# Optimization experiments

Measured on AMD Instinct MI355X. Metric: run time of the kernel, lower is better.

Reference implementation:

```python
import jax, jax.numpy as jnp
import numpy as np

N, E, D, L = 100000, 400000, 300, 5
BN_EPS = 1e-5


def setup_inputs() -> dict:
    key = jax.random.key(0)
    ks = jax.random.split(key, 8)
    x = jax.random.randint(ks[0], (N, 7), 0, 5)
    edge_index = jax.random.randint(ks[1], (2, E), 0, N)
    edge_attr = jax.random.randint(ks[2], (E, 4), 0, 2)
    s = 0.1
    atom_tables = jax.random.normal(ks[3], (7, 119, D), jnp.float32) * s
    bond_tables = jax.random.normal(ks[4], (L, 4, 6, D), jnp.float32) * s
    mlp_w1 = jax.random.normal(ks[5], (L, D, 2 * D), jnp.float32) * (1.0 / np.sqrt(D))
    mlp_b1 = jnp.zeros((L, 2 * D), jnp.float32)
    mlp_w2 = jax.random.normal(ks[6], (L, 2 * D, D), jnp.float32) * (1.0 / np.sqrt(2 * D))
    mlp_b2 = jnp.zeros((L, D), jnp.float32)
    bn_gamma = jnp.ones((L, D), jnp.float32)
    bn_beta = jnp.zeros((L, D), jnp.float32)
    return dict(x=x, edge_index=edge_index, edge_attr=edge_attr,
                atom_tables=atom_tables, bond_tables=bond_tables,
                mlp_w1=mlp_w1, mlp_b1=mlp_b1, mlp_w2=mlp_w2, mlp_b2=mlp_b2,
                bn_gamma=bn_gamma, bn_beta=bn_beta)


def reference(x, edge_index, edge_attr, atom_tables, bond_tables,
              mlp_w1, mlp_b1, mlp_w2, mlp_b2, bn_gamma, bn_beta):
    n = x.shape[0]
    # add self loops (PyG add_self_loops appends them)
    loop = jnp.arange(n)
    src = jnp.concatenate([edge_index[0], loop])  # message source j
    dst = jnp.concatenate([edge_index[1], loop])  # aggregation target i
    self_loop_attr = jnp.zeros((n, 4), edge_attr.dtype).at[:, 0].set(4)
    ea = jnp.concatenate([edge_attr, self_loop_attr], axis=0)  # [E+N, 4]

    # AtomEncoder: sum of 7 per-feature embeddings -> [N, D]
    h = atom_tables[jnp.arange(7), x].sum(axis=1)

    for l in range(L):
        # BondEncoder: sum of 4 per-feature embeddings -> [E+N, D]
        e_emb = bond_tables[l][jnp.arange(4), ea].sum(axis=1)
        # GIN message = x_j + edge_emb, aggr='add' by target node
        msg = h[src] + e_emb
        agg = jax.ops.segment_sum(msg, dst, num_segments=n)
        # GIN update MLP: Linear -> ReLU -> Linear
        hid = jax.nn.relu(agg @ mlp_w1[l] + mlp_b1[l])
        out = hid @ mlp_w2[l] + mlp_b2[l]
        # BatchNorm1d (training mode: batch stats, biased var)
        mu = out.mean(axis=0)
        var = out.var(axis=0)
        out = (out - mu) / jnp.sqrt(var + BN_EPS) * bn_gamma[l] + bn_beta[l]
        # drop_ratio = 0.0 -> dropout is identity; ReLU except last layer
        if l < L - 1:
            out = jax.nn.relu(out)
        h = out
    return h  # JK='last'
```

## Files before the change

kernel.cpp:

```cpp
#include <hip/hip_runtime.h>

typedef unsigned short u16;
typedef unsigned int   u32;
typedef __bf16 bf16x8 __attribute__((ext_vector_type(8)));
typedef float  f32x4  __attribute__((ext_vector_type(4)));

__device__ __forceinline__ u16 f2bf(float f) {
    u32 u = __builtin_bit_cast(u32, f);
    u = u + 0x7fffu + ((u >> 16) & 1u);
    return (u16)(u >> 16);
}
__device__ __forceinline__ float bflo(u32 u) { return __builtin_bit_cast(float, u << 16); }
__device__ __forceinline__ float bfhi(u32 u) { return __builtin_bit_cast(float, u & 0xffff0000u); }
__device__ __forceinline__ u32 pack2(float x, float y) { return (u32)f2bf(x) | ((u32)f2bf(y) << 16); }

#define NN 100000
#define EE 400000
#define DP 320
#define HP 640

__global__ void count_deg(const int* __restrict__ ei, int* __restrict__ deg, int E) {
    int e = blockIdx.x * 256 + threadIdx.x;
    if (e < E) atomicAdd(&deg[ei[E + e]], 1);
}

__global__ void scan1(const int* __restrict__ deg, int* __restrict__ out, int* __restrict__ bsums, int n) {
    __shared__ int lds[1024];
    int t = threadIdx.x;
    int i = blockIdx.x * 1024 + t;
    int v = (i < n) ? deg[i] : 0;
    lds[t] = v;
    __syncthreads();
    for (int d = 1; d < 1024; d <<= 1) {
        int add = (t >= d) ? lds[t - d] : 0;
        __syncthreads();
        lds[t] += add;
        __syncthreads();
    }
    if (i < n) out[i] = lds[t] - v;
    if (t == 1023) bsums[blockIdx.x] = lds[t];
}

__global__ void scan2(int* __restrict__ bsums, int nb) {
    __shared__ int lds[128];
    int t = threadIdx.x;
    int v = (t < nb) ? bsums[t] : 0;
    lds[t] = v;
    __syncthreads();
    for (int d = 1; d < 128; d <<= 1) {
        int add = (t >= d) ? lds[t - d] : 0;
        __syncthreads();
        lds[t] += add;
        __syncthreads();
    }
    if (t < nb) bsums[t] = lds[t] - v;
}

__global__ void scan3(int* __restrict__ out, const int* __restrict__ bsums, int n, int etot) {
    int i = blockIdx.x * 1024 + threadIdx.x;
    if (i < n) out[i] += bsums[blockIdx.x];
    else if (i == n) out[i] = etot;
}

__global__ void fill_csr(const int* __restrict__ ei, const int* __restrict__ ea,
                         int* __restrict__ cursors, u32* __restrict__ vals, int E) {
    int e = blockIdx.x * 256 + threadIdx.x;
    if (e >= E) return;
    int dst = ei[E + e];
    int src = ei[e];
    u32 code = (u32)((ea[e*4] & 1) | ((ea[e*4+1] & 1) << 1) | ((ea[e*4+2] & 1) << 2) | ((ea[e*4+3] & 1) << 3));
    int pos = atomicAdd(&cursors[dst], 1);
    vals[pos] = ((u32)src << 4) | code;
}

__global__ void conv_w1(const float* __restrict__ w, u16* __restrict__ wt) {
    int id = blockIdx.x * 256 + threadIdx.x;
    if (id >= 5 * HP * DP) return;
    int l = id / (HP * DP);
    int rem = id - l * (HP * DP);
    int n = rem / DP;
    int k = rem - n * DP;
    u16 v = 0;
    if (n < 600 && k < 300) v = f2bf(w[((size_t)l * 300 + k) * 600 + n]);
    wt[id] = v;
}
__global__ void conv_w2(const float* __restrict__ w, u16* __restrict__ wt) {
    int id = blockIdx.x * 256 + threadIdx.x;
    if (id >= 5 * DP * HP) return;
    int l = id / (DP * HP);
    int rem = id - l * (DP * HP);
    int n = rem / HP;
    int k = rem - n * HP;
    u16 v = 0;
    if (n < 300 && k < 600) v = f2bf(w[((size_t)l * 600 + k) * 300 + n]);
    wt[id] = v;
}

__global__ void atom_enc(const int* __restrict__ x, const float* __restrict__ at, u16* __restrict__ y) {
    const int i = blockIdx.x;
    const int d = threadIdx.x;
    __shared__ int xi[7];
    if (d < 7) xi[d] = x[i * 7 + d];
    __syncthreads();
    u16 v = 0;
    if (d < 300) {
        float s = 0.f;
        #pragma unroll
        for (int f = 0; f < 7; ++f) s += at[(f * 119 + xi[f]) * 300 + d];
        v = f2bf(s);
    }
    y[(size_t)i * DP + d] = v;
}

__global__ void bond_enc(const float* __restrict__ bt, float* __restrict__ emb) {
    const int c = blockIdx.x;
    const int d = threadIdx.x;
    float s = 0.f;
    if (d < 300) {
        if (c < 16) {
            #pragma unroll
            for (int f = 0; f < 4; ++f) s += bt[(f * 6 + ((c >> f) & 1)) * 300 + d];
        } else {
            s = bt[4 * 300 + d];
            #pragma unroll
            for (int f = 1; f < 4; ++f) s += bt[f * 6 * 300 + d];
        }
    }
    emb[c * DP + d] = s;
}

__global__ void bn_ss(const float* __restrict__ stats, const float* __restrict__ gamma,
                      const float* __restrict__ beta, float* __restrict__ scale,
                      float* __restrict__ shift, int n) {
    int d = threadIdx.x;
    float sc = 0.f, sh = 0.f;
    if (d < 300) {
        float inv_n = 1.0f / (float)n;
        float mu = stats[d] * inv_n;
        float var = stats[DP + d] * inv_n - mu * mu;
        float inv = 1.0f / sqrtf(var + 1e-5f);
        sc = gamma[d] * inv;
        sh = beta[d] - mu * sc;
    }
    scale[d] = sc; shift[d] = sh;
}

__global__ void bn_apply(const float* __restrict__ hraw, const float* __restrict__ scale,
                         const float* __restrict__ shift, u16* __restrict__ y) {
    const int i = blockIdx.x;
    const int d = threadIdx.x;
    float v = fmaf(scale[d], hraw[(size_t)i * DP + d], shift[d]);
    y[(size_t)i * DP + d] = f2bf(fmaxf(v, 0.f));
}

__global__ void aggregate(const u16* __restrict__ y,
                          const float* __restrict__ emb,
                          const int* __restrict__ offs, const u32* __restrict__ vals,
                          u16* __restrict__ agg, const int n) {
    const int wid = (int)((blockIdx.x * (size_t)blockDim.x + threadIdx.x) >> 6);
    const int lane = threadIdx.x & 63;
    if (wid >= n) return;
    const int j0 = lane, j1 = lane + 64, j2 = lane + 128;
    const bool has2 = (lane < 32);

    float a0x = 0.f, a0y = 0.f, a1x = 0.f, a1y = 0.f, a2x = 0.f, a2y = 0.f;

    auto accum = [&](int srcrow, const float* erow) {
        const u32* row = (const u32*)y + (size_t)srcrow * (DP / 2);
        u32 u0 = row[j0], u1 = row[j1];
        u32 u2 = has2 ? row[j2] : 0u;
        float2 e0 = *(const float2*)(erow + 2 * j0);
        float2 e1 = *(const float2*)(erow + 2 * j1);
        a0x += bflo(u0) + e0.x;  a0y += bfhi(u0) + e0.y;
        a1x += bflo(u1) + e1.x;  a1y += bfhi(u1) + e1.y;
        if (has2) {
            float2 e2 = *(const float2*)(erow + 2 * j2);
            a2x += bflo(u2) + e2.x;  a2y += bfhi(u2) + e2.y;
        }
    };

    accum(wid, emb + 16 * DP);
    const int s = offs[wid], t = offs[wid + 1];
    for (int e = s; e < t; ++e) {
        u32 v = vals[e];
        accum((int)(v >> 4), emb + (v & 15u) * DP);
    }

    u32* out = (u32*)agg + (size_t)wid * (DP / 2);
    out[j0] = pack2(a0x, a0y);
    out[j1] = pack2(a1x, a1y);
    if (has2) out[j2] = pack2(a2x, a2y);
}

#define ASTR 328
#define HSTR 40

__global__ __launch_bounds__(512, 2) void fused_mlp(
    const u16* __restrict__ A,
    const u16* __restrict__ W1t,
    const u16* __restrict__ W2t,
    const float* __restrict__ b1g,
    const float* __restrict__ b2g,
    float* __restrict__ H,
    float* __restrict__ st1, float* __restrict__ st2,
    const int M) {

    __shared__ __align__(16) u16 As[128 * ASTR];
    __shared__ __align__(16) u16 Wb[2][320 * HSTR];
    __shared__ __align__(16) u16 hidT[128 * HSTR];

    const int tid  = threadIdx.x;
    const int bm   = blockIdx.x * 128;
    const int wave = tid >> 6;
    const int lane = tid & 63;
    const int mg   = wave >> 1;
    const int ng   = wave & 1;
    const int l15  = lane & 15;
    const int q    = lane >> 4;

    #pragma unroll
    for (int it = 0; it < 10; ++it) {
        int u = tid + it * 512;
        int row = u / 40, ku = u - row * 40;
        uint4 v; v.x = v.y = v.z = v.w = 0;
        if (bm + row < M) v = *(const uint4*)(A + (size_t)(bm + row) * DP + ku * 8);
        *(uint4*)&As[row * ASTR + ku * 8] = v;
    }
    {
        uint4 w0 = *(const uint4*)(W1t + (size_t)(tid / 40) * DP + (tid % 40) * 8);
        uint4 w1v = *(const uint4*)(W1t + (size_t)((tid + 512) / 40) * DP + ((tid + 512) % 40) * 8);
        uint4 w2v; w2v.x = w2v.y = w2v.z = w2v.w = 0;
        int u2 = tid + 1024;
        if (u2 < 1280) w2v = *(const uint4*)(W1t + (size_t)(u2 / 40) * DP + (u2 % 40) * 8);
        *(uint4*)&Wb[0][(tid / 40) * ASTR + (tid % 40) * 8] = w0;
        *(uint4*)&Wb[0][((tid + 512) / 40) * ASTR + ((tid + 512) % 40) * 8] = w1v;
        if (u2 < 1280) *(uint4*)&Wb[0][(u2 / 40) * ASTR + (u2 % 40) * 8] = w2v;
    }
    __syncthreads();

    bf16x8 afr[2][10];
    #pragma unroll
    for (int mf = 0; mf < 2; ++mf)
        #pragma unroll
        for (int kt = 0; kt < 10; ++kt) {
            uint4 t = *(const uint4*)&As[(mg * 32 + mf * 16 + l15) * ASTR + kt * 32 + q * 8];
            afr[mf][kt] = __builtin_bit_cast(bf16x8, t);
        }

    f32x4 acc2[2][10];
    const f32x4 zero4 = {0.f, 0.f, 0.f, 0.f};
    #pragma unroll
    for (int mf = 0; mf < 2; ++mf)
        #pragma unroll
        for (int nf = 0; nf < 10; ++nf) acc2[mf][nf] = zero4;

    for (int c = 0; c < 20; ++c) {
        uint4 p0, p1, p2;
        {
            int u0 = tid, u1 = tid + 512, u2 = tid + 1024;
            p0 = *(const uint4*)(W2t + (size_t)(u0 >> 2) * HP + c * 32 + (u0 & 3) * 8);
            p1 = *(const uint4*)(W2t + (size_t)(u1 >> 2) * HP + c * 32 + (u1 & 3) * 8);
            p2.x = p2.y = p2.z = p2.w = 0;
            if (u2 < 1280) p2 = *(const uint4*)(W2t + (size_t)(u2 >> 2) * HP + c * 32 + (u2 & 3) * 8);
        }

        f32x4 acc1[2] = {zero4, zero4};
        #pragma unroll
        for (int kt = 0; kt < 10; ++kt) {
            uint4 t = *(const uint4*)&Wb[0][(ng * 16 + l15) * ASTR + kt * 32 + q * 8];
            bf16x8 bfr = __builtin_bit_cast(bf16x8, t);
            acc1[0] = __builtin_amdgcn_mfma_f32_16x16x32_bf16(afr[0][kt], bfr, acc1[0], 0, 0, 0);
            acc1[1] = __builtin_amdgcn_mfma_f32_16x16x32_bf16(afr[1][kt], bfr, acc1[1], 0, 0, 0);
        }
        {
            int gcol = c * 32 + ng * 16 + l15;
            float bb = (gcol < 600) ? b1g[gcol] : 0.f;
            #pragma unroll
            for (int mf = 0; mf < 2; ++mf)
                #pragma unroll
                for (int r = 0; r < 4; ++r) {
                    float v = fmaxf(acc1[mf][r] + bb, 0.f);
                    hidT[(mg * 32 + mf * 16 + q * 4 + r) * HSTR + ng * 16 + l15] = f2bf(v);
                }
        }
        {
            int u0 = tid, u1 = tid + 512, u2 = tid + 1024;
            *(uint4*)&Wb[1][(u0 >> 2) * HSTR + (u0 & 3) * 8] = p0;
            *(uint4*)&Wb[1][(u1 >> 2) * HSTR + (u1 & 3) * 8] = p1;
            if (u2 < 1280) *(uint4*)&Wb[1][(u2 >> 2) * HSTR + (u2 & 3) * 8] = p2;
        }
        __syncthreads();

        uint4 q0, q1, q2;
        if (c < 19) {
            int u0 = tid, u1 = tid + 512, u2 = tid + 1024;
            const u16* base = W1t + (size_t)(c + 1) * 32 * DP;
            q0 = *(const uint4*)(base + (size_t)(u0 / 40) * DP + (u0 % 40) * 8);
            q1 = *(const uint4*)(base + (size_t)(u1 / 40) * DP + (u1 % 40) * 8);
            q2.x = q2.y = q2.z = q2.w = 0;
            if (u2 < 1280) q2 = *(const uint4*)(base + (size_t)(u2 / 40) * DP + (u2 % 40) * 8);
        }

        bf16x8 a2[2];
        #pragma unroll
        for (int mf = 0; mf < 2; ++mf) {
            uint4 t = *(const uint4*)&hidT[(mg * 32 + mf * 16 + l15) * HSTR + q * 8];
            a2[mf] = __builtin_bit_cast(bf16x8, t);
        }
        #pragma unroll
        for (int nf = 0; nf < 10; ++nf) {
            uint4 t = *(const uint4*)&Wb[1][(ng * 160 + nf * 16 + l15) * HSTR + q * 8];
            bf16x8 bfr = __builtin_bit_cast(bf16x8, t);
            acc2[0][nf] = __builtin_amdgcn_mfma_f32_16x16x32_bf16(a2[0], bfr, acc2[0][nf], 0, 0, 0);
            acc2[1][nf] = __builtin_amdgcn_mfma_f32_16x16x32_bf16(a2[1], bfr, acc2[1][nf], 0, 0, 0);
        }

        if (c < 19) {
            int u0 = tid, u1 = tid + 512, u2 = tid + 1024;
            *(uint4*)&Wb[0][(u0 / 40) * ASTR + (u0 % 40) * 8] = q0;
            *(uint4*)&Wb[0][(u1 / 40) * ASTR + (u1 % 40) * 8] = q1;
            if (u2 < 1280) *(uint4*)&Wb[0][(u2 / 40) * ASTR + (u2 % 40) * 8] = q2;
        }
        __syncthreads();
    }

    #pragma unroll
    for (int nf = 0; nf < 10; ++nf) {
        const int col = ng * 160 + nf * 16 + l15;
        const float bb = (col < 300) ? b2g[col] : 0.f;
        float s1 = 0.f, s2 = 0.f;
        #pragma unroll
        for (int mf = 0; mf < 2; ++mf)
            #pragma unroll
            for (int r = 0; r < 4; ++r) {
                const int row = bm + mg * 32 + mf * 16 + q * 4 + r;
                if (row < M) {
                    float v = acc2[mf][nf][r] + bb;
                    H[(size_t)row * DP + col] = v;
                    s1 += v; s2 += v * v;
                }
            }
        s1 += __shfl_xor(s1, 16); s1 += __shfl_xor(s1, 32);
        s2 += __shfl_xor(s2, 16); s2 += __shfl_xor(s2, 32);
        if (q == 0) { atomicAdd(&st1[col], s1); atomicAdd(&st2[col], s2); }
    }
}

__global__ void finalize(const float* __restrict__ hraw, const float* __restrict__ scale,
                         const float* __restrict__ shift, float* __restrict__ out) {
    const int i = blockIdx.x;
    const int d = threadIdx.x;
    if (d < 300) {
        float x = hraw[(size_t)i * DP + d];
        out[(size_t)i * 300 + d] = fmaf(scale[d], x, shift[d]);
    }
}

extern "C" void kernel_launch(void* const* d_in, const int* in_sizes, int n_in,
                              void* d_out, int out_size, void* d_ws, size_t ws_size,
                              hipStream_t stream) {
    const int N = NN, E = EE, L = 5;
    const int*   x     = (const int*)d_in[0];
    const int*   ei    = (const int*)d_in[1];
    const int*   ea    = (const int*)d_in[2];
    const float* at    = (const float*)d_in[3];
    const float* bt    = (const float*)d_in[4];
    const float* w1    = (const float*)d_in[5];
    const float* b1    = (const float*)d_in[6];
    const float* w2    = (const float*)d_in[7];
    const float* b2    = (const float*)d_in[8];
    const float* gamma = (const float*)d_in[9];
    const float* beta  = (const float*)d_in[10];
    float* out = (float*)d_out;

    char* ws = (char*)d_ws;
    size_t off = 0;
    auto alloc = [&](size_t bytes) { char* p = ws + off; off = (off + bytes + 255) & ~(size_t)255; return p; };
    u16* buf_y    = (u16*)alloc((size_t)N * DP * 2);
    u16* buf_agg  = (u16*)alloc((size_t)N * DP * 2);
    float* buf_h  = (float*)alloc((size_t)N * DP * 4);
    u16* w1t      = (u16*)alloc((size_t)5 * HP * DP * 2);
    u16* w2t      = (u16*)alloc((size_t)5 * DP * HP * 2);
    int* deg      = (int*)alloc((size_t)N * 4);
    int* offs     = (int*)alloc((size_t)(N + 1) * 4);
    int* cursors  = (int*)alloc((size_t)N * 4);
    u32* vals     = (u32*)alloc((size_t)E * 4);
    int* bsums    = (int*)alloc(128 * 4);
    float* emb    = (float*)alloc(17 * DP * 4);
    float* stats  = (float*)alloc(2 * DP * 4);
    float* scale  = (float*)alloc(DP * 4);
    float* shift  = (float*)alloc(DP * 4);

    (void)hipMemsetAsync(deg, 0, (size_t)N * 4, stream);
    count_deg<<<(E + 255) / 256, 256, 0, stream>>>(ei, deg, E);
    const int nb = (N + 1023) / 1024;
    scan1<<<nb, 1024, 0, stream>>>(deg, offs, bsums, N);
    scan2<<<1, 128, 0, stream>>>(bsums, nb);
    scan3<<<(N + 1 + 1023) / 1024, 1024, 0, stream>>>(offs, bsums, N, E);
    (void)hipMemcpyAsync(cursors, offs, (size_t)N * 4, hipMemcpyDeviceToDevice, stream);
    fill_csr<<<(E + 255) / 256, 256, 0, stream>>>(ei, ea, cursors, vals, E);

    conv_w1<<<(5 * HP * DP + 255) / 256, 256, 0, stream>>>(w1, w1t);
    conv_w2<<<(5 * DP * HP + 255) / 256, 256, 0, stream>>>(w2, w2t);

    atom_enc<<<N, DP, 0, stream>>>(x, at, buf_y);

    const int MB = (N + 127) / 128;
    for (int l = 0; l < L; ++l) {
        bond_enc<<<17, DP, 0, stream>>>(bt + (size_t)l * 4 * 6 * 300, emb);
        aggregate<<<(N * 64 + 255) / 256, 256, 0, stream>>>(
            buf_y, emb, offs, vals, buf_agg, N);
        (void)hipMemsetAsync(stats, 0, 2 * DP * 4, stream);
        fused_mlp<<<MB, 512, 0, stream>>>(
            buf_agg,
            w1t + (size_t)l * HP * DP, w2t + (size_t)l * DP * HP,
            b1 + (size_t)l * 600, b2 + (size_t)l * 300,
            buf_h, stats, stats + DP, N);
        bn_ss<<<1, DP, 0, stream>>>(stats, gamma + (size_t)l * 300, beta + (size_t)l * 300, scale, shift, N);
        if (l < L - 1)
            bn_apply<<<N, DP, 0, stream>>>(buf_h, scale, shift, buf_y);
    }
    finalize<<<N, DP, 0, stream>>>(buf_h, scale, shift, out);
}
```

Baseline: 2.134 ms.

## Load A fragments directly from global and shrink LDS to raise MLP occupancy

```diff
diff --git a/kernel.cpp b/kernel.cpp
--- a/kernel.cpp
+++ b/kernel.cpp
@@ -193,9 +193,8 @@
 }
 
 #define ASTR 328
-#define HSTR 40
-
-__global__ __launch_bounds__(512, 2) void fused_mlp(
+
+__global__ __launch_bounds__(512, 6) void fused_mlp(
     const u16* __restrict__ A,
     const u16* __restrict__ W1t,
     const u16* __restrict__ W2t,
@@ -205,9 +204,9 @@
     float* __restrict__ st1, float* __restrict__ st2,
     const int M) {
 
-    __shared__ __align__(16) u16 As[128 * ASTR];
-    __shared__ __align__(16) u16 Wb[2][320 * HSTR];
-    __shared__ __align__(16) u16 hidT[128 * HSTR];
+    __shared__ __align__(16) u16 Wb0[32 * ASTR];
+    __shared__ __align__(16) u16 Wb1[320 * 32];
+    __shared__ __align__(16) u16 hidT[128 * 32];
 
     const int tid  = threadIdx.x;
     const int bm   = blockIdx.x * 128;
@@ -218,34 +217,27 @@
     const int l15  = lane & 15;
     const int q    = lane >> 4;
 
-    #pragma unroll
-    for (int it = 0; it < 10; ++it) {
-        int u = tid + it * 512;
-        int row = u / 40, ku = u - row * 40;
-        uint4 v; v.x = v.y = v.z = v.w = 0;
-        if (bm + row < M) v = *(const uint4*)(A + (size_t)(bm + row) * DP + ku * 8);
-        *(uint4*)&As[row * ASTR + ku * 8] = v;
-    }
     {
-        uint4 w0 = *(const uint4*)(W1t + (size_t)(tid / 40) * DP + (tid % 40) * 8);
-        uint4 w1v = *(const uint4*)(W1t + (size_t)((tid + 512) / 40) * DP + ((tid + 512) % 40) * 8);
+        int u0 = tid, u1 = tid + 512, u2 = tid + 1024;
+        uint4 w0  = *(const uint4*)(W1t + (size_t)(u0 / 40) * DP + (u0 % 40) * 8);
+        uint4 w1v = *(const uint4*)(W1t + (size_t)(u1 / 40) * DP + (u1 % 40) * 8);
         uint4 w2v; w2v.x = w2v.y = w2v.z = w2v.w = 0;
-        int u2 = tid + 1024;
         if (u2 < 1280) w2v = *(const uint4*)(W1t + (size_t)(u2 / 40) * DP + (u2 % 40) * 8);
-        *(uint4*)&Wb[0][(tid / 40) * ASTR + (tid % 40) * 8] = w0;
-        *(uint4*)&Wb[0][((tid + 512) / 40) * ASTR + ((tid + 512) % 40) * 8] = w1v;
-        if (u2 < 1280) *(uint4*)&Wb[0][(u2 / 40) * ASTR + (u2 % 40) * 8] = w2v;
-    }
-    __syncthreads();
+        *(uint4*)&Wb0[(u0 / 40) * ASTR + (u0 % 40) * 8] = w0;
+        *(uint4*)&Wb0[(u1 / 40) * ASTR + (u1 % 40) * 8] = w1v;
+        if (u2 < 1280) *(uint4*)&Wb0[(u2 / 40) * ASTR + (u2 % 40) * 8] = w2v;
+    }
 
     bf16x8 afr[2][10];
     #pragma unroll
-    for (int mf = 0; mf < 2; ++mf)
-        #pragma unroll
-        for (int kt = 0; kt < 10; ++kt) {
-            uint4 t = *(const uint4*)&As[(mg * 32 + mf * 16 + l15) * ASTR + kt * 32 + q * 8];
-            afr[mf][kt] = __builtin_bit_cast(bf16x8, t);
-        }
+    for (int mf = 0; mf < 2; ++mf) {
+        int row = bm + mg * 32 + mf * 16 + l15;
+        if (row > M - 1) row = M - 1;
+        const u16* ap = A + (size_t)row * DP + q * 8;
+        #pragma unroll
+        for (int kt = 0; kt < 10; ++kt)
+            afr[mf][kt] = __builtin_bit_cast(bf16x8, *(const uint4*)(ap + kt * 32));
+    }
 
     f32x4 acc2[2][10];
     const f32x4 zero4 = {0.f, 0.f, 0.f, 0.f};
@@ -253,6 +245,8 @@
     for (int mf = 0; mf < 2; ++mf)
         #pragma unroll
         for (int nf = 0; nf < 10; ++nf) acc2[mf][nf] = zero4;
+
+    __syncthreads();
 
     for (int c = 0; c < 20; ++c) {
         uint4 p0, p1, p2;
@@ -267,7 +261,7 @@
         f32x4 acc1[2] = {zero4, zero4};
         #pragma unroll
         for (int kt = 0; kt < 10; ++kt) {
-            uint4 t = *(const uint4*)&Wb[0][(ng * 16 + l15) * ASTR + kt * 32 + q * 8];
+            uint4 t = *(const uint4*)&Wb0[(ng * 16 + l15) * ASTR + kt * 32 + q * 8];
             bf16x8 bfr = __builtin_bit_cast(bf16x8, t);
             acc1[0] = __builtin_amdgcn_mfma_f32_16x16x32_bf16(afr[0][kt], bfr, acc1[0], 0, 0, 0);
             acc1[1] = __builtin_amdgcn_mfma_f32_16x16x32_bf16(afr[1][kt], bfr, acc1[1], 0, 0, 0);
@@ -280,14 +274,16 @@
                 #pragma unroll
                 for (int r = 0; r < 4; ++r) {
                     float v = fmaxf(acc1[mf][r] + bb, 0.f);
-                    hidT[(mg * 32 + mf * 16 + q * 4 + r) * HSTR + ng * 16 + l15] = f2bf(v);
+                    int row = mg * 32 + mf * 16 + q * 4 + r;
+                    int sb  = ((ng * 2 + (l15 >> 3)) ^ ((row >> 2) & 3)) * 8 + (l15 & 7);
+                    hidT[row * 32 + sb] = f2bf(v);
                 }
         }
         {
             int u0 = tid, u1 = tid + 512, u2 = tid + 1024;
-            *(uint4*)&Wb[1][(u0 >> 2) * HSTR + (u0 & 3) * 8] = p0;
-            *(uint4*)&Wb[1][(u1 >> 2) * HSTR + (u1 & 3) * 8] = p1;
-            if (u2 < 1280) *(uint4*)&Wb[1][(u2 >> 2) * HSTR + (u2 & 3) * 8] = p2;
+            *(uint4*)&Wb1[u0 * 8] = p0;
+            *(uint4*)&Wb1[u1 * 8] = p1;
+            if (u2 < 1280) *(uint4*)&Wb1[u2 * 8] = p2;
         }
         __syncthreads();
 
@@ -304,12 +300,14 @@
         bf16x8 a2[2];
         #pragma unroll
         for (int mf = 0; mf < 2; ++mf) {
-            uint4 t = *(const uint4*)&hidT[(mg * 32 + mf * 16 + l15) * HSTR + q * 8];
+            int rr = mg * 32 + mf * 16 + l15;
+            int sblk = q ^ ((rr >> 2) & 3);
+            uint4 t = *(const uint4*)&hidT[rr * 32 + sblk * 8];
             a2[mf] = __builtin_bit_cast(bf16x8, t);
         }
         #pragma unroll
         for (int nf = 0; nf < 10; ++nf) {
-            uint4 t = *(const uint4*)&Wb[1][(ng * 160 + nf * 16 + l15) * HSTR + q * 8];
+            uint4 t = *(const uint4*)&Wb1[(ng * 160 + nf * 16 + l15) * 32 + q * 8];
             bf16x8 bfr = __builtin_bit_cast(bf16x8, t);
             acc2[0][nf] = __builtin_amdgcn_mfma_f32_16x16x32_bf16(a2[0], bfr, acc2[0][nf], 0, 0, 0);
             acc2[1][nf] = __builtin_amdgcn_mfma_f32_16x16x32_bf16(a2[1], bfr, acc2[1][nf], 0, 0, 0);
@@ -317,9 +315,9 @@
 
         if (c < 19) {
             int u0 = tid, u1 = tid + 512, u2 = tid + 1024;
-            *(uint4*)&Wb[0][(u0 / 40) * ASTR + (u0 % 40) * 8] = q0;
-            *(uint4*)&Wb[0][(u1 / 40) * ASTR + (u1 % 40) * 8] = q1;
-            if (u2 < 1280) *(uint4*)&Wb[0][(u2 / 40) * ASTR + (u2 % 40) * 8] = q2;
+            *(uint4*)&Wb0[(u0 / 40) * ASTR + (u0 % 40) * 8] = q0;
+            *(uint4*)&Wb0[(u1 / 40) * ASTR + (u1 % 40) * 8] = q1;
+            if (u2 < 1280) *(uint4*)&Wb0[(u2 / 40) * ASTR + (u2 % 40) * 8] = q2;
         }
         __syncthreads();
     }
```

New measurement: 6.445 ms. 202% more time.
